# Kernel optimization log

Hardware: AMD Instinct MI355X
Metric: run time of the kernel (lower is better)

Reference implementation:

```python
import jax, jax.numpy as jnp
import numpy as np

H = 64          # hidden_dim
L = 4           # num_layers
N_SENS = 32
OUT_DIM = 3
EPS = 1e-5


def _ln(x, g, b):
    m = jnp.mean(x, axis=-1, keepdims=True)
    v = jnp.var(x, axis=-1, keepdims=True)
    return (x - m) / jnp.sqrt(v + EPS) * g + b


def _gelu(x):
    return jax.nn.gelu(x, approximate=False)  # torch nn.GELU default (erf)


def setup_inputs() -> dict:
    key = jax.random.key(0)
    ks = jax.random.split(key, 12)
    B, T = 512, 2048
    s = 0.05
    return {
        "sensors": jax.random.normal(ks[0], (B, T, N_SENS), dtype=jnp.float32),
        # input_proj: Linear(n_sensors,H), LayerNorm(H), GELU, Linear(H,H)
        "W_in1": jax.random.normal(ks[1], (N_SENS, H), dtype=jnp.float32) * s,
        "b_in1": jnp.zeros((H,), jnp.float32),
        "ln1_g": jnp.ones((H,), jnp.float32),
        "ln1_b": jnp.zeros((H,), jnp.float32),
        "W_in2": jax.random.normal(ks[2], (H, H), dtype=jnp.float32) * s,
        "b_in2": jnp.zeros((H,), jnp.float32),
        # stacked LSTM cell gate weights: Linear(2H, 4H) per layer
        "Wg": jax.random.normal(ks[3], (L, 2 * H, 4 * H), dtype=jnp.float32) * s,
        "bg": jnp.zeros((L, 4 * H), jnp.float32),
        # output_proj: LayerNorm(H), Linear(H,H), GELU, Linear(H,out)
        "ln2_g": jnp.ones((H,), jnp.float32),
        "ln2_b": jnp.zeros((H,), jnp.float32),
        "W_out1": jax.random.normal(ks[4], (H, H), dtype=jnp.float32) * s,
        "b_out1": jnp.zeros((H,), jnp.float32),
        "W_out2": jax.random.normal(ks[5], (H, OUT_DIM), dtype=jnp.float32) * s,
        "b_out2": jnp.zeros((OUT_DIM,), jnp.float32),
    }


def _forward(sensors, W_in1, b_in1, ln1_g, ln1_b, W_in2, b_in2,
             Wg, bg, ln2_g, ln2_b, W_out1, b_out1, W_out2, b_out2):
    B, T, _ = sensors.shape
    # input projection (batched over B,T)
    x = _gelu(_ln(sensors @ W_in1 + b_in1, ln1_g, ln1_b)) @ W_in2 + b_in2  # [B,T,H]
    x_t = jnp.swapaxes(x, 0, 1)  # [T,B,H] for scan over time

    h0 = jnp.zeros((L, B, H), x.dtype)
    c0 = jnp.zeros((L, B, H), x.dtype)

    def step(carry, xt):
        h, c = carry  # [L,B,H]
        inp = xt
        hs, cs = [], []
        for l in range(L):  # fixed small layer loop
            combined = jnp.concatenate([inp, h[l]], axis=-1)  # [B,2H]
            gates = combined @ Wg[l] + bg[l]                   # [B,4H]
            i, f, g, o = jnp.split(gates, 4, axis=-1)
            c_new = jax.nn.sigmoid(f) * c[l] + jax.nn.sigmoid(i) * jnp.tanh(g)
            h_new = jax.nn.sigmoid(o) * jnp.tanh(c_new)
            hs.append(h_new)
            cs.append(c_new)
            inp = h_new
        return (jnp.stack(hs), jnp.stack(cs)), hs[-1]

    _, out_t = jax.lax.scan(step, (h0, c0), x_t)  # out_t: [T,B,H]
    out = jnp.swapaxes(out_t, 0, 1)  # [B,T,H]
    y = _gelu(_ln(out, ln2_g, ln2_b) @ W_out1 + b_out1) @ W_out2 + b_out2
    return y  # [B,T,OUT_DIM]


def reference(sensors, W_in1, b_in1, ln1_g, ln1_b, W_in2, b_in2,
              Wg, bg, ln2_g, ln2_b, W_out1, b_out1, W_out2, b_out2):
    return _forward(sensors, W_in1, b_in1, ln1_g, ln1_b, W_in2, b_in2,
                    Wg, bg, ln2_g, ln2_b, W_out1, b_out1, W_out2, b_out2)
```

## Files before the change

kernel.cpp:

```cpp
#include <hip/hip_runtime.h>
#include <math.h>

#define B_   512
#define T_   2048
#define H_   64
#define NS_  32
#define HH_  128
#define G4_  256
#define EPSF 1e-5f

typedef _Float16 half8 __attribute__((ext_vector_type(8)));
typedef _Float16 h4   __attribute__((ext_vector_type(4)));
typedef float    f32x4 __attribute__((ext_vector_type(4)));

__device__ __forceinline__ float gelu_f(float x) {
    return 0.5f * x * (1.0f + erff(x * 0.70710678118654752440f));
}
__device__ __forceinline__ float sigmoid_f(float x) {
    return 1.0f / (1.0f + __expf(-x));
}
__device__ __forceinline__ float tanh_f(float x) {
    return 1.0f - 2.0f / (__expf(2.0f * x) + 1.0f);
}

__global__ void __launch_bounds__(256) inproj_kernel(
    const float* __restrict__ sensors, const float* __restrict__ W1,
    const float* __restrict__ b1, const float* __restrict__ g1,
    const float* __restrict__ bb1, const float* __restrict__ W2,
    const float* __restrict__ b2, _Float16* __restrict__ seqh)
{
    __shared__ __align__(16) float W1l[NS_ * H_];
    __shared__ __align__(16) float W2l[H_ * H_];
    __shared__ float p1[H_], p2[H_], p3[H_], p4[H_];
    const int tid = threadIdx.x;
    {
        const float4* s1 = (const float4*)W1;
        float4* d1 = (float4*)W1l;
        for (int i = tid; i < NS_ * H_ / 4; i += 256) d1[i] = s1[i];
        const float4* s2 = (const float4*)W2;
        float4* d2 = (float4*)W2l;
        for (int i = tid; i < H_ * H_ / 4; i += 256) d2[i] = s2[i];
        if (tid < H_) { p1[tid] = b1[tid]; p2[tid] = g1[tid];
                        p3[tid] = bb1[tid]; p4[tid] = b2[tid]; }
    }
    __syncthreads();

    const long idx = (long)blockIdx.x * 256 + tid;
    const float* srow = sensors + idx * NS_;
    float sv[NS_];
    #pragma unroll
    for (int q = 0; q < NS_ / 4; ++q) {
        float4 v = *(const float4*)&srow[q * 4];
        sv[q*4+0] = v.x; sv[q*4+1] = v.y; sv[q*4+2] = v.z; sv[q*4+3] = v.w;
    }
    float t1[H_];
    #pragma unroll
    for (int jb = 0; jb < H_ / 4; ++jb) {
        float ax = p1[jb*4+0], ay = p1[jb*4+1], az = p1[jb*4+2], aw = p1[jb*4+3];
        #pragma unroll
        for (int k = 0; k < NS_; ++k) {
            float4 w = *(const float4*)&W1l[k * H_ + jb * 4];
            ax += sv[k]*w.x; ay += sv[k]*w.y; az += sv[k]*w.z; aw += sv[k]*w.w;
        }
        t1[jb*4+0] = ax; t1[jb*4+1] = ay; t1[jb*4+2] = az; t1[jb*4+3] = aw;
    }
    float mean = 0.f;
    #pragma unroll
    for (int j = 0; j < H_; ++j) mean += t1[j];
    mean *= (1.0f / H_);
    float var = 0.f;
    #pragma unroll
    for (int j = 0; j < H_; ++j) { float d = t1[j] - mean; var += d * d; }
    var *= (1.0f / H_);
    const float inv = rsqrtf(var + EPSF);
    #pragma unroll
    for (int j = 0; j < H_; ++j) {
        float nv = (t1[j] - mean) * inv * p2[j] + p3[j];
        t1[j] = gelu_f(nv);
    }
    _Float16* orow = seqh + idx * H_;
    for (int ob = 0; ob < H_ / 4; ++ob) {
        float ax = p4[ob*4+0], ay = p4[ob*4+1];
        float az = p4[ob*4+2], aw = p4[ob*4+3];
        #pragma unroll
        for (int j = 0; j < H_; ++j) {
            float4 w = *(const float4*)&W2l[j * H_ + ob * 4];
            ax += t1[j]*w.x; ay += t1[j]*w.y; az += t1[j]*w.z; aw += t1[j]*w.w;
        }
        h4 o; o[0] = (_Float16)ax; o[1] = (_Float16)ay;
              o[2] = (_Float16)az; o[3] = (_Float16)aw;
        *(h4*)&orow[ob * 4] = o;
    }
}

__global__ void __launch_bounds__(512, 2) lstm_fused_kernel(
    const float* __restrict__ Wg, const float* __restrict__ bg,
    const _Float16* __restrict__ xin,
    _Float16* __restrict__ h3f16,
    float* __restrict__ h3f32)
{
    __shared__ __align__(16) char combB[4 * 16 * 256];
    __shared__ __align__(8)  float gbuf[4][G4_][2];

    const int tid  = threadIdx.x;
    const int wv   = tid >> 6;
    const int lane = tid & 63;
    const int l    = wv >> 1;
    const int half = wv & 1;
    const int nlayer = tid >> 7;
    const int nrow   = (tid >> 6) & 1;
    const int u      = tid & 63;

    const float* W = Wg + (size_t)l * HH_ * G4_;
    half8 wf[4][8];
    #pragma unroll
    for (int kt = 0; kt < 4; ++kt) {
        #pragma unroll
        for (int nt = 0; nt < 8; ++nt) {
            half8 f;
            #pragma unroll
            for (int j = 0; j < 8; ++j) {
                const int k   = kt * 32 + (lane >> 4) * 8 + j;
                const int col = half * 128 + nt * 16 + (lane & 15);
                f[j] = (_Float16)W[k * G4_ + col];
            }
            wf[kt][nt] = f;
        }
    }

    const float* bgp = bg + nlayer * G4_;
    const float bi = bgp[u], bff = bgp[64 + u], bgg = bgp[128 + u], bo = bgp[192 + u];
    const long nrowbase = ((long)(blockIdx.x * 2 + nrow)) * T_ * H_;

    for (int i = tid; i < 4 * 16 * 256 / 4; i += 512) ((float*)combB)[i] = 0.f;
    __syncthreads();
    if (nlayer == 0) {
        const _Float16 x0 = xin[nrowbase + u];
        const int byte = nrow * 256 + ((2 * u) ^ ((nrow & 7) << 4));
        *(_Float16*)(combB + byte) = x0;
    }
    __syncthreads();

    float c_reg = 0.f;
    const int arow  = lane & 15;
    const int kgrp  = (lane >> 4) * 16;
    const int abase = l * 4096 + arow * 256;
    const int axor  = (arow & 7) << 4;

    for (int s = 0; s < T_ + 3; ++s) {
        const bool mact = (s >= l) && (s - l < T_);
        const bool nact = (s >= nlayer) && (s - nlayer < T_);
        _Float16 xnext = (_Float16)0.f;
        if (nlayer == 0 && s + 1 < T_)
            xnext = xin[nrowbase + (long)(s + 1) * H_ + u];

        if (mact) {
            half8 af[4];
            #pragma unroll
            for (int kt = 0; kt < 4; ++kt) {
                const int byte = abase + ((kt * 64 + kgrp) ^ axor);
                af[kt] = *(const half8*)(combB + byte);
            }
            f32x4 acc[8];
            #pragma unroll
            for (int nt = 0; nt < 8; ++nt) acc[nt] = (f32x4){0.f, 0.f, 0.f, 0.f};
            #pragma unroll
            for (int kt = 0; kt < 4; ++kt) {
                #pragma unroll
                for (int nt = 0; nt < 8; ++nt)
                    acc[nt] = __builtin_amdgcn_mfma_f32_16x16x32_f16(
                        af[kt], wf[kt][nt], acc[nt], 0, 0, 0);
            }
            if (lane < 16) {
                #pragma unroll
                for (int nt = 0; nt < 8; ++nt) {
                    const int col = half * 128 + nt * 16 + lane;
                    float2 r; r.x = acc[nt][0]; r.y = acc[nt][1];
                    *(float2*)&gbuf[l][col][0] = r;
                }
            }
        }
        __syncthreads();
        if (nact) {
            const int t = s - nlayer;
            const float gi = gbuf[nlayer][u][nrow]       + bi;
            const float gf = gbuf[nlayer][64 + u][nrow]  + bff;
            const float gg = gbuf[nlayer][128 + u][nrow] + bgg;
            const float go = gbuf[nlayer][192 + u][nrow] + bo;
            c_reg = sigmoid_f(gf) * c_reg + sigmoid_f(gi) * tanh_f(gg);
            const float hn = sigmoid_f(go) * tanh_f(c_reg);
            const _Float16 hh = (_Float16)hn;
            const int hb = nlayer * 4096 + nrow * 256 + ((128 + 2 * u) ^ ((nrow & 7) << 4));
            *(_Float16*)(combB + hb) = hh;
            if (nlayer < 3) {
                const int xb = (nlayer + 1) * 4096 + nrow * 256 + ((2 * u) ^ ((nrow & 7) << 4));
                *(_Float16*)(combB + xb) = hh;
            } else if (h3f32) h3f32[nrowbase + (long)t * H_ + u] = hn;
              else            h3f16[nrowbase + (long)t * H_ + u] = hh;
            if (nlayer == 0 && s + 1 < T_) {
                const int xb = nrow * 256 + ((2 * u) ^ ((nrow & 7) << 4));
                *(_Float16*)(combB + xb) = xnext;
            }
        }
        __syncthreads();
    }
}

__global__ void __launch_bounds__(256) outproj_kernel(
    const _Float16* __restrict__ h16, const float* __restrict__ h32, int use32,
    const float* __restrict__ g2, const float* __restrict__ b2,
    const float* __restrict__ W1, const float* __restrict__ b1,
    const float* __restrict__ W2, const float* __restrict__ b2o,
    float* __restrict__ y)
{
    __shared__ __align__(16) float W1l[H_ * H_];
    __shared__ __align__(16) float W2l[H_ * 4];
    __shared__ float pg[H_], pb[H_], pb1[H_];
    const int tid = threadIdx.x;
    {
        const float4* s1 = (const float4*)W1;
        float4* d1 = (float4*)W1l;
        for (int i = tid; i < H_ * H_ / 4; i += 256) d1[i] = s1[i];
        if (tid < H_) {
            pg[tid] = g2[tid]; pb[tid] = b2[tid]; pb1[tid] = b1[tid];
            float4 w; w.x = W2[tid*3+0]; w.y = W2[tid*3+1]; w.z = W2[tid*3+2]; w.w = 0.f;
            *(float4*)&W2l[tid * 4] = w;
        }
    }
    __syncthreads();

    const long idx = (long)blockIdx.x * 256 + tid;
    float hv[H_];
    if (use32) {
        const float* hrow = h32 + idx * H_;
        #pragma unroll
        for (int q = 0; q < H_ / 4; ++q) {
            float4 v = *(const float4*)&hrow[q * 4];
            hv[q*4+0] = v.x; hv[q*4+1] = v.y; hv[q*4+2] = v.z; hv[q*4+3] = v.w;
        }
    } else {
        const _Float16* hrow = h16 + idx * H_;
        #pragma unroll
        for (int q = 0; q < H_ / 8; ++q) {
            half8 v = *(const half8*)&hrow[q * 8];
            #pragma unroll
            for (int j = 0; j < 8; ++j) hv[q*8+j] = (float)v[j];
        }
    }
    float mean = 0.f;
    #pragma unroll
    for (int j = 0; j < H_; ++j) mean += hv[j];
    mean *= (1.0f / H_);
    float var = 0.f;
    #pragma unroll
    for (int j = 0; j < H_; ++j) { float dd = hv[j] - mean; var += dd * dd; }
    var *= (1.0f / H_);
    const float inv = rsqrtf(var + EPSF);
    #pragma unroll
    for (int j = 0; j < H_; ++j) hv[j] = (hv[j] - mean) * inv * pg[j] + pb[j];

    float y0 = b2o[0], y1 = b2o[1], y2 = b2o[2];
    for (int ob = 0; ob < H_ / 4; ++ob) {
        float ax = pb1[ob*4+0], ay = pb1[ob*4+1];
        float az = pb1[ob*4+2], aw = pb1[ob*4+3];
        #pragma unroll
        for (int j = 0; j < H_; ++j) {
            float4 w = *(const float4*)&W1l[j * H_ + ob * 4];
            ax += hv[j]*w.x; ay += hv[j]*w.y; az += hv[j]*w.z; aw += hv[j]*w.w;
        }
        ax = gelu_f(ax); ay = gelu_f(ay); az = gelu_f(az); aw = gelu_f(aw);
        float4 wa = *(const float4*)&W2l[(ob*4+0) * 4];
        float4 wb = *(const float4*)&W2l[(ob*4+1) * 4];
        float4 wc = *(const float4*)&W2l[(ob*4+2) * 4];
        float4 wd = *(const float4*)&W2l[(ob*4+3) * 4];
        y0 += ax*wa.x + ay*wb.x + az*wc.x + aw*wd.x;
        y1 += ax*wa.y + ay*wb.y + az*wc.y + aw*wd.y;
        y2 += ax*wa.z + ay*wb.z + az*wc.z + aw*wd.z;
    }
    y[idx * 3 + 0] = y0;
    y[idx * 3 + 1] = y1;
    y[idx * 3 + 2] = y2;
}

extern "C" void kernel_launch(void* const* d_in, const int* in_sizes, int n_in,
                              void* d_out, int out_size, void* d_ws, size_t ws_size,
                              hipStream_t stream)
{
    const float* sensors = (const float*)d_in[0];
    const float* W_in1   = (const float*)d_in[1];
    const float* b_in1   = (const float*)d_in[2];
    const float* ln1_g   = (const float*)d_in[3];
    const float* ln1_b   = (const float*)d_in[4];
    const float* W_in2   = (const float*)d_in[5];
    const float* b_in2   = (const float*)d_in[6];
    const float* Wg      = (const float*)d_in[7];
    const float* bg      = (const float*)d_in[8];
    const float* ln2_g   = (const float*)d_in[9];
    const float* ln2_b   = (const float*)d_in[10];
    const float* W_out1  = (const float*)d_in[11];
    const float* b_out1  = (const float*)d_in[12];
    const float* W_out2  = (const float*)d_in[13];
    const float* b_out2  = (const float*)d_in[14];
    float* y = (float*)d_out;

    const size_t elems = (size_t)B_ * T_ * H_;
    _Float16* seqh = (_Float16*)d_ws;
    float* h3f32 = nullptr;
    int use32 = 0;
    if (ws_size >= elems * 2 + elems * 4) {
        h3f32 = (float*)((char*)d_ws + elems * 2);
        use32 = 1;
    }

    inproj_kernel<<<B_ * T_ / 256, 256, 0, stream>>>(
        sensors, W_in1, b_in1, ln1_g, ln1_b, W_in2, b_in2, seqh);
    lstm_fused_kernel<<<B_ / 2, 512, 0, stream>>>(Wg, bg, seqh, seqh, h3f32);
    outproj_kernel<<<B_ * T_ / 256, 256, 0, stream>>>(
        seqh, h3f32, use32, ln2_g, ln2_b, W_out1, b_out1, W_out2, b_out2, y);
}
```

Before: 3.171 ms.

## Compute LSTM gate activations in MFMA lanes with double-buffered state, one barrier per step

Gate columns are remapped so each wave's MFMA output holds matching i/f/g/o columns for its units. The pointwise LSTM update can then run directly on the accumulators instead of going through a shared gate buffer. The combined input/hidden buffer is double-buffered by step parity, which removes one of the two __syncthreads per timestep. Bias is folded into the accumulator init. The trade-off is that only 16 lanes per wave do the pointwise work, each handling 4 units serially, and rows 2-15 of the A operand are zero-padded.

```diff
diff --git a/kernel.cpp b/kernel.cpp
--- a/kernel.cpp
+++ b/kernel.cpp
@@ -93,115 +93,132 @@
     }
 }
 
+#define CIDX(p,l,r,k) ((((p)*4 + (l))*2 + (r))*128 + (k))
+
 __global__ void __launch_bounds__(512, 2) lstm_fused_kernel(
     const float* __restrict__ Wg, const float* __restrict__ bg,
     const _Float16* __restrict__ xin,
     _Float16* __restrict__ h3f16,
     float* __restrict__ h3f32)
 {
-    __shared__ __align__(16) char combB[4 * 16 * 256];
-    __shared__ __align__(8)  float gbuf[4][G4_][2];
+    __shared__ __align__(16) _Float16 combh[2 * 4 * 2 * HH_];
 
     const int tid  = threadIdx.x;
     const int wv   = tid >> 6;
     const int lane = tid & 63;
     const int l    = wv >> 1;
-    const int half = wv & 1;
-    const int nlayer = tid >> 7;
-    const int nrow   = (tid >> 6) & 1;
-    const int u      = tid & 63;
+    const int h_   = wv & 1;
+    const int L    = lane & 15;
+    const int kgrp = lane >> 4;
+    const int arow = L;
 
     const float* W = Wg + (size_t)l * HH_ * G4_;
     half8 wf[4][8];
     #pragma unroll
     for (int kt = 0; kt < 4; ++kt) {
         #pragma unroll
-        for (int nt = 0; nt < 8; ++nt) {
+        for (int a = 0; a < 8; ++a) {
+            const int col = (a >> 1) * 64 + h_ * 32 + (a & 1) * 16 + L;
             half8 f;
             #pragma unroll
-            for (int j = 0; j < 8; ++j) {
-                const int k   = kt * 32 + (lane >> 4) * 8 + j;
-                const int col = half * 128 + nt * 16 + (lane & 15);
-                f[j] = (_Float16)W[k * G4_ + col];
-            }
-            wf[kt][nt] = f;
-        }
-    }
-
-    const float* bgp = bg + nlayer * G4_;
-    const float bi = bgp[u], bff = bgp[64 + u], bgg = bgp[128 + u], bo = bgp[192 + u];
-    const long nrowbase = ((long)(blockIdx.x * 2 + nrow)) * T_ * H_;
-
-    for (int i = tid; i < 4 * 16 * 256 / 4; i += 512) ((float*)combB)[i] = 0.f;
+            for (int j = 0; j < 8; ++j)
+                f[j] = (_Float16)W[(kt * 32 + kgrp * 8 + j) * G4_ + col];
+            wf[kt][a] = f;
+        }
+    }
+    float ba[8];
+    #pragma unroll
+    for (int a = 0; a < 8; ++a)
+        ba[a] = bg[l * G4_ + (a >> 1) * 64 + h_ * 32 + (a & 1) * 16 + L];
+
+    const int  u0 = h_ * 32 + L, u1 = u0 + 16;
+    const long rb0 = ((long)(blockIdx.x * 2 + 0)) * T_ * H_;
+    const long rb1 = ((long)(blockIdx.x * 2 + 1)) * T_ * H_;
+    const int  xrow = lane >> 5;
+    const int  xu   = h_ * 32 + (lane & 31);
+    const long xbase = ((long)(blockIdx.x * 2 + xrow)) * T_ * H_ + xu;
+
+    for (int i = tid; i < 2 * 4 * 2 * HH_ / 2; i += 512)
+        ((float*)combh)[i] = 0.f;
     __syncthreads();
-    if (nlayer == 0) {
-        const _Float16 x0 = xin[nrowbase + u];
-        const int byte = nrow * 256 + ((2 * u) ^ ((nrow & 7) << 4));
-        *(_Float16*)(combB + byte) = x0;
-    }
+    if (l == 0) combh[CIDX(0, 0, xrow, xu)] = xin[xbase];
     __syncthreads();
 
-    float c_reg = 0.f;
-    const int arow  = lane & 15;
-    const int kgrp  = (lane >> 4) * 16;
-    const int abase = l * 4096 + arow * 256;
-    const int axor  = (arow & 7) << 4;
+    float c00 = 0.f, c01 = 0.f, c10 = 0.f, c11 = 0.f;
 
     for (int s = 0; s < T_ + 3; ++s) {
-        const bool mact = (s >= l) && (s - l < T_);
-        const bool nact = (s >= nlayer) && (s - nlayer < T_);
+        const int p = s & 1, q = p ^ 1;
+        const bool act = (s >= l) && (s - l < T_);
+
         _Float16 xnext = (_Float16)0.f;
-        if (nlayer == 0 && s + 1 < T_)
-            xnext = xin[nrowbase + (long)(s + 1) * H_ + u];
-
-        if (mact) {
+        if (l == 0 && s + 1 < T_)
+            xnext = xin[xbase + (long)(s + 1) * H_];
+
+        if (act) {
             half8 af[4];
             #pragma unroll
             for (int kt = 0; kt < 4; ++kt) {
-                const int byte = abase + ((kt * 64 + kgrp) ^ axor);
-                af[kt] = *(const half8*)(combB + byte);
+                half8 v = {};
+                if (arow < 2)
+                    v = *(const half8*)&combh[CIDX(p, l, arow, kt * 32 + kgrp * 8)];
+                af[kt] = v;
             }
             f32x4 acc[8];
             #pragma unroll
-            for (int nt = 0; nt < 8; ++nt) acc[nt] = (f32x4){0.f, 0.f, 0.f, 0.f};
+            for (int a = 0; a < 8; ++a)
+                acc[a] = (f32x4){ba[a], ba[a], ba[a], ba[a]};
             #pragma unroll
             for (int kt = 0; kt < 4; ++kt) {
                 #pragma unroll
-                for (int nt = 0; nt < 8; ++nt)
-                    acc[nt] = __builtin_amdgcn_mfma_f32_16x16x32_f16(
-                        af[kt], wf[kt][nt], acc[nt], 0, 0, 0);
+                for (int a = 0; a < 8; ++a)
+                    acc[a] = __builtin_amdgcn_mfma_f32_16x16x32_f16(
+                        af[kt], wf[kt][a], acc[a], 0, 0, 0);
             }
+
             if (lane < 16) {
-                #pragma unroll
-                for (int nt = 0; nt < 8; ++nt) {
-                    const int col = half * 128 + nt * 16 + lane;
-                    float2 r; r.x = acc[nt][0]; r.y = acc[nt][1];
-                    *(float2*)&gbuf[l][col][0] = r;
+                const int t = s - l;
+                const float i00 = sigmoid_f(acc[0][0]), f00 = sigmoid_f(acc[2][0]);
+                const float g00 = tanh_f(acc[4][0]),    o00 = sigmoid_f(acc[6][0]);
+                const float i01 = sigmoid_f(acc[0][1]), f01 = sigmoid_f(acc[2][1]);
+                const float g01 = tanh_f(acc[4][1]),    o01 = sigmoid_f(acc[6][1]);
+                const float i10 = sigmoid_f(acc[1][0]), f10 = sigmoid_f(acc[3][0]);
+                const float g10 = tanh_f(acc[5][0]),    o10 = sigmoid_f(acc[7][0]);
+                const float i11 = sigmoid_f(acc[1][1]), f11 = sigmoid_f(acc[3][1]);
+                const float g11 = tanh_f(acc[5][1]),    o11 = sigmoid_f(acc[7][1]);
+                c00 = f00 * c00 + i00 * g00;
+                c01 = f01 * c01 + i01 * g01;
+                c10 = f10 * c10 + i10 * g10;
+                c11 = f11 * c11 + i11 * g11;
+                const float h00 = o00 * tanh_f(c00);
+                const float h01 = o01 * tanh_f(c01);
+                const float h10 = o10 * tanh_f(c10);
+                const float h11 = o11 * tanh_f(c11);
+                const _Float16 q00 = (_Float16)h00, q01 = (_Float16)h01;
+                const _Float16 q10 = (_Float16)h10, q11 = (_Float16)h11;
+                combh[CIDX(q, l, 0, 64 + u0)] = q00;
+                combh[CIDX(q, l, 1, 64 + u0)] = q01;
+                combh[CIDX(q, l, 0, 64 + u1)] = q10;
+                combh[CIDX(q, l, 1, 64 + u1)] = q11;
+                if (l < 3) {
+                    combh[CIDX(q, l + 1, 0, u0)] = q00;
+                    combh[CIDX(q, l + 1, 1, u0)] = q01;
+                    combh[CIDX(q, l + 1, 0, u1)] = q10;
+                    combh[CIDX(q, l + 1, 1, u1)] = q11;
+                } else if (h3f32) {
+                    h3f32[rb0 + (long)t * H_ + u0] = h00;
+                    h3f32[rb1 + (long)t * H_ + u0] = h01;
+                    h3f32[rb0 + (long)t * H_ + u1] = h10;
+                    h3f32[rb1 + (long)t * H_ + u1] = h11;
+                } else {
+                    h3f16[rb0 + (long)t * H_ + u0] = q00;
+                    h3f16[rb1 + (long)t * H_ + u0] = q01;
+                    h3f16[rb0 + (long)t * H_ + u1] = q10;
+                    h3f16[rb1 + (long)t * H_ + u1] = q11;
                 }
             }
         }
-        __syncthreads();
-        if (nact) {
-            const int t = s - nlayer;
-            const float gi = gbuf[nlayer][u][nrow]       + bi;
-            const float gf = gbuf[nlayer][64 + u][nrow]  + bff;
-            const float gg = gbuf[nlayer][128 + u][nrow] + bgg;
-            const float go = gbuf[nlayer][192 + u][nrow] + bo;
-            c_reg = sigmoid_f(gf) * c_reg + sigmoid_f(gi) * tanh_f(gg);
-            const float hn = sigmoid_f(go) * tanh_f(c_reg);
-            const _Float16 hh = (_Float16)hn;
-            const int hb = nlayer * 4096 + nrow * 256 + ((128 + 2 * u) ^ ((nrow & 7) << 4));
-            *(_Float16*)(combB + hb) = hh;
-            if (nlayer < 3) {
-                const int xb = (nlayer + 1) * 4096 + nrow * 256 + ((2 * u) ^ ((nrow & 7) << 4));
-                *(_Float16*)(combB + xb) = hh;
-            } else if (h3f32) h3f32[nrowbase + (long)t * H_ + u] = hn;
-              else            h3f16[nrowbase + (long)t * H_ + u] = hh;
-            if (nlayer == 0 && s + 1 < T_) {
-                const int xb = nrow * 256 + ((2 * u) ^ ((nrow & 7) << 4));
-                *(_Float16*)(combB + xb) = xnext;
-            }
-        }
+        if (l == 0 && s + 1 < T_)
+            combh[CIDX(q, 0, xrow, xu)] = xnext;
         __syncthreads();
     }
 }
```

After: 4.471 ms (median of 5 runs). 41.0% more time.

## Shrink LSTM shared buffers, fold gate bias into MFMA init, write fp16 final hidden

Applied to the files above, without the earlier changes.

The LSTM kernel's LDS staging shrinks from a 16-row padded swizzled A tile to a compact 2-row buffer, with MFMA A fragments read by lane parity. Gate biases are preloaded into the MFMA accumulators, which removes the per-step bias adds in the elementwise phase. The x-input prefetch is spread across both layer-0 waves. The final-layer output is always written as fp16 to a separate buffer, dropping the fp32 path, which halves the writes from the LSTM and the reads in the output projection but lowers precision of the last hidden state. It also assumes the workspace holds two fp16 sequences without checking ws_size.

```diff
diff --git a/kernel.cpp b/kernel.cpp
--- a/kernel.cpp
+++ b/kernel.cpp
@@ -96,20 +96,18 @@
 __global__ void __launch_bounds__(512, 2) lstm_fused_kernel(
     const float* __restrict__ Wg, const float* __restrict__ bg,
     const _Float16* __restrict__ xin,
-    _Float16* __restrict__ h3f16,
-    float* __restrict__ h3f32)
+    _Float16* __restrict__ h3out)
 {
-    __shared__ __align__(16) char combB[4 * 16 * 256];
-    __shared__ __align__(8)  float gbuf[4][G4_][2];
+    __shared__ __align__(16) _Float16 combh[4][2][HH_];
+    __shared__ __align__(8)  float gbuf[4][4][H_][2];
 
     const int tid  = threadIdx.x;
     const int wv   = tid >> 6;
     const int lane = tid & 63;
     const int l    = wv >> 1;
     const int half = wv & 1;
-    const int nlayer = tid >> 7;
-    const int nrow   = (tid >> 6) & 1;
-    const int u      = tid & 63;
+    const int L    = lane & 15;
+    const int kgrp = lane >> 4;
 
     const float* W = Wg + (size_t)l * HH_ * G4_;
     half8 wf[4][8];
@@ -117,53 +115,54 @@
     for (int kt = 0; kt < 4; ++kt) {
         #pragma unroll
         for (int nt = 0; nt < 8; ++nt) {
+            const int col = half * 128 + nt * 16 + L;
             half8 f;
             #pragma unroll
-            for (int j = 0; j < 8; ++j) {
-                const int k   = kt * 32 + (lane >> 4) * 8 + j;
-                const int col = half * 128 + nt * 16 + (lane & 15);
-                f[j] = (_Float16)W[k * G4_ + col];
-            }
+            for (int j = 0; j < 8; ++j)
+                f[j] = (_Float16)W[(kt * 32 + kgrp * 8 + j) * G4_ + col];
             wf[kt][nt] = f;
         }
     }
-
-    const float* bgp = bg + nlayer * G4_;
-    const float bi = bgp[u], bff = bgp[64 + u], bgg = bgp[128 + u], bo = bgp[192 + u];
-    const long nrowbase = ((long)(blockIdx.x * 2 + nrow)) * T_ * H_;
-
-    for (int i = tid; i < 4 * 16 * 256 / 4; i += 512) ((float*)combB)[i] = 0.f;
+    float ba[8];
+    #pragma unroll
+    for (int nt = 0; nt < 8; ++nt)
+        ba[nt] = bg[l * G4_ + half * 128 + nt * 16 + L];
+
+    const int nl_l = tid >> 7;
+    const int nrow = (tid >> 6) & 1;
+    const int u    = tid & 63;
+    const long nbase = ((long)(blockIdx.x * 2 + nrow)) * T_ * H_ + u;
+
+    const int  xrow = lane >> 5;
+    const int  xu   = half * 32 + (lane & 31);
+    const long xbase = ((long)(blockIdx.x * 2 + xrow)) * T_ * H_ + xu;
+
+    for (int i = tid; i < 4 * 2 * HH_ / 2; i += 512) ((float*)combh)[i] = 0.f;
     __syncthreads();
-    if (nlayer == 0) {
-        const _Float16 x0 = xin[nrowbase + u];
-        const int byte = nrow * 256 + ((2 * u) ^ ((nrow & 7) << 4));
-        *(_Float16*)(combB + byte) = x0;
-    }
+    if (l == 0) combh[0][xrow][xu] = xin[xbase];
     __syncthreads();
 
     float c_reg = 0.f;
-    const int arow  = lane & 15;
-    const int kgrp  = (lane >> 4) * 16;
-    const int abase = l * 4096 + arow * 256;
-    const int axor  = (arow & 7) << 4;
 
     for (int s = 0; s < T_ + 3; ++s) {
         const bool mact = (s >= l) && (s - l < T_);
-        const bool nact = (s >= nlayer) && (s - nlayer < T_);
+        const bool nact = (s >= nl_l) && (s - nl_l < T_);
+
         _Float16 xnext = (_Float16)0.f;
-        if (nlayer == 0 && s + 1 < T_)
-            xnext = xin[nrowbase + (long)(s + 1) * H_ + u];
+        if (l == 0 && s + 1 < T_)
+            xnext = xin[xbase + (long)(s + 1) * H_];
 
         if (mact) {
+            const _Float16* cp = &combh[l][lane & 1][0];
             half8 af[4];
             #pragma unroll
-            for (int kt = 0; kt < 4; ++kt) {
-                const int byte = abase + ((kt * 64 + kgrp) ^ axor);
-                af[kt] = *(const half8*)(combB + byte);
-            }
+            for (int kt = 0; kt < 4; ++kt)
+                af[kt] = *(const half8*)&cp[kt * 32 + kgrp * 8];
+
             f32x4 acc[8];
             #pragma unroll
-            for (int nt = 0; nt < 8; ++nt) acc[nt] = (f32x4){0.f, 0.f, 0.f, 0.f};
+            for (int nt = 0; nt < 8; ++nt)
+                acc[nt] = (f32x4){ba[nt], ba[nt], ba[nt], ba[nt]};
             #pragma unroll
             for (int kt = 0; kt < 4; ++kt) {
                 #pragma unroll
@@ -175,39 +174,36 @@
                 #pragma unroll
                 for (int nt = 0; nt < 8; ++nt) {
                     const int col = half * 128 + nt * 16 + lane;
-                    float2 r; r.x = acc[nt][0]; r.y = acc[nt][1];
-                    *(float2*)&gbuf[l][col][0] = r;
+                    const int g   = col >> 6;
+                    const int ug  = col & 63;
+                    float2 v; v.x = acc[nt][0]; v.y = acc[nt][1];
+                    *(float2*)&gbuf[l][g][ug][0] = v;
                 }
             }
         }
         __syncthreads();
+
         if (nact) {
-            const int t = s - nlayer;
-            const float gi = gbuf[nlayer][u][nrow]       + bi;
-            const float gf = gbuf[nlayer][64 + u][nrow]  + bff;
-            const float gg = gbuf[nlayer][128 + u][nrow] + bgg;
-            const float go = gbuf[nlayer][192 + u][nrow] + bo;
+            const int t = s - nl_l;
+            const float gi = gbuf[nl_l][0][u][nrow];
+            const float gf = gbuf[nl_l][1][u][nrow];
+            const float gg = gbuf[nl_l][2][u][nrow];
+            const float go = gbuf[nl_l][3][u][nrow];
             c_reg = sigmoid_f(gf) * c_reg + sigmoid_f(gi) * tanh_f(gg);
             const float hn = sigmoid_f(go) * tanh_f(c_reg);
             const _Float16 hh = (_Float16)hn;
-            const int hb = nlayer * 4096 + nrow * 256 + ((128 + 2 * u) ^ ((nrow & 7) << 4));
-            *(_Float16*)(combB + hb) = hh;
-            if (nlayer < 3) {
-                const int xb = (nlayer + 1) * 4096 + nrow * 256 + ((2 * u) ^ ((nrow & 7) << 4));
-                *(_Float16*)(combB + xb) = hh;
-            } else if (h3f32) h3f32[nrowbase + (long)t * H_ + u] = hn;
-              else            h3f16[nrowbase + (long)t * H_ + u] = hh;
-            if (nlayer == 0 && s + 1 < T_) {
-                const int xb = nrow * 256 + ((2 * u) ^ ((nrow & 7) << 4));
-                *(_Float16*)(combB + xb) = xnext;
-            }
-        }
+            combh[nl_l][nrow][64 + u] = hh;
+            if (nl_l < 3) combh[nl_l + 1][nrow][u] = hh;
+            else          h3out[nbase + (long)t * H_] = hh;
+        }
+        if (l == 0 && s + 1 < T_)
+            combh[0][xrow][xu] = xnext;
         __syncthreads();
     }
 }
 
 __global__ void __launch_bounds__(256) outproj_kernel(
-    const _Float16* __restrict__ h16, const float* __restrict__ h32, int use32,
+    const _Float16* __restrict__ h16,
     const float* __restrict__ g2, const float* __restrict__ b2,
     const float* __restrict__ W1, const float* __restrict__ b1,
     const float* __restrict__ W2, const float* __restrict__ b2o,
@@ -230,22 +226,13 @@
     __syncthreads();
 
     const long idx = (long)blockIdx.x * 256 + tid;
+    const _Float16* hrow = h16 + idx * H_;
     float hv[H_];
-    if (use32) {
-        const float* hrow = h32 + idx * H_;
-        #pragma unroll
-        for (int q = 0; q < H_ / 4; ++q) {
-            float4 v = *(const float4*)&hrow[q * 4];
-            hv[q*4+0] = v.x; hv[q*4+1] = v.y; hv[q*4+2] = v.z; hv[q*4+3] = v.w;
-        }
-    } else {
-        const _Float16* hrow = h16 + idx * H_;
-        #pragma unroll
-        for (int q = 0; q < H_ / 8; ++q) {
-            half8 v = *(const half8*)&hrow[q * 8];
-            #pragma unroll
-            for (int j = 0; j < 8; ++j) hv[q*8+j] = (float)v[j];
-        }
+    #pragma unroll
+    for (int q = 0; q < H_ / 8; ++q) {
+        half8 v = *(const half8*)&hrow[q * 8];
+        #pragma unroll
+        for (int j = 0; j < 8; ++j) hv[q*8+j] = (float)v[j];
     }
     float mean = 0.f;
     #pragma unroll
@@ -305,16 +292,11 @@
 
     const size_t elems = (size_t)B_ * T_ * H_;
     _Float16* seqh = (_Float16*)d_ws;
-    float* h3f32 = nullptr;
-    int use32 = 0;
-    if (ws_size >= elems * 2 + elems * 4) {
-        h3f32 = (float*)((char*)d_ws + elems * 2);
-        use32 = 1;
-    }
+    _Float16* h3   = (_Float16*)((char*)d_ws + elems * 2);
 
     inproj_kernel<<<B_ * T_ / 256, 256, 0, stream>>>(
         sensors, W_in1, b_in1, ln1_g, ln1_b, W_in2, b_in2, seqh);
-    lstm_fused_kernel<<<B_ / 2, 512, 0, stream>>>(Wg, bg, seqh, seqh, h3f32);
+    lstm_fused_kernel<<<B_ / 2, 512, 0, stream>>>(Wg, bg, seqh, h3);
     outproj_kernel<<<B_ * T_ / 256, 256, 0, stream>>>(
-        seqh, h3f32, use32, ln2_g, ln2_b, W_out1, b_out1, W_out2, b_out2, y);
-}
+        h3, ln2_g, ln2_b, W_out1, b_out1, W_out2, b_out2, y);
+}
```

Result: faster. 3.082 ms (-2.8%).
